# Optimization experiments

Measured on AMD Instinct MI355X. Metric: run time of the kernel, lower is better.

The kernel has to match this reference:

```python
import jax, jax.numpy as jnp
import numpy as np

HEADS = 16
EPS = 1e-6

def _rmsnorm(x, g):
    # x: (..., d); norm = ||x||_2 * d^-0.5 (matches torch.norm-based RMSNorm)
    d = x.shape[-1]
    nrm = jnp.linalg.norm(x, axis=-1, keepdims=True) * (d ** -0.5)
    return x / (nrm + EPS) * g

def _rope(x, cos, sin):
    # x: (b,n,h,d) -> complex pairs over last dim; cos/sin: (1,n,1,d//2)
    b, n, h, d = x.shape
    xr = x.reshape(b, n, h, d // 2, 2)
    re, im = xr[..., 0], xr[..., 1]
    out_re = re * cos - im * sin
    out_im = re * sin + im * cos
    return jnp.stack([out_re, out_im], axis=-1).reshape(b, n, h, d)

def setup_inputs() -> dict:
    key = jax.random.key(0)
    ks = jax.random.split(key, 8)
    b, n, dim = 4, 4096, 1024
    d = dim // HEADS
    x = jax.random.normal(ks[0], (b, n, dim), dtype=jnp.float32)
    # rope freqs as cos/sin of random angles (broadcast shape 1,n,1,d//2)
    ang = jax.random.uniform(ks[1], (1, n, 1, d // 2), dtype=jnp.float32) * (2 * np.pi)
    freqs_cos = jnp.cos(ang)
    freqs_sin = jnp.sin(ang)
    sc = dim ** -0.5
    w_qkv = jax.random.normal(ks[2], (dim, 3 * dim), dtype=jnp.float32) * sc
    g_q = jnp.ones((d,), dtype=jnp.float32)
    g_k = jnp.ones((d,), dtype=jnp.float32)
    w_proj = jax.random.normal(ks[3], (dim, dim), dtype=jnp.float32) * sc
    b_proj = jnp.zeros((dim,), dtype=jnp.float32)
    return {"x": x, "freqs_cos": freqs_cos, "freqs_sin": freqs_sin,
            "w_qkv": w_qkv, "g_q": g_q, "g_k": g_k,
            "w_proj": w_proj, "b_proj": b_proj}

def reference(x, freqs_cos, freqs_sin, w_qkv, g_q, g_k, w_proj, b_proj):
    b, n, dim = x.shape
    h = HEADS
    d = dim // h
    scale = d ** -0.5
    qkv = x @ w_qkv  # (b,n,3*dim)
    q, k, v = jnp.split(qkv, 3, axis=-1)
    q = q.reshape(b, n, h, d)
    k = k.reshape(b, n, h, d)
    v = v.reshape(b, n, h, d)
    q = _rmsnorm(q, g_q)
    k = _rmsnorm(k, g_k)
    q = _rope(q, freqs_cos, freqs_sin)
    k = _rope(k, freqs_cos, freqs_sin)
    # per-token head-mixing attention: (b,n,h,h)
    attn = jnp.einsum('bnhd,bngd->bnhg', q, k) * scale
    attn = jax.nn.softmax(attn, axis=-1)
    out = jnp.einsum('bnhg,bngd->bnhd', attn, v).reshape(b, n, dim)
    return out @ w_proj + b_proj
```

## Files before the change

kernel.cpp:

```cpp
#include <hip/hip_runtime.h>
#include <hip/hip_bf16.h>
#include <stddef.h>

#define NTOK   16384
#define SEQN   4096
#define DIM    1024
#define K3     3072
#define HEADS  16
#define HD     64

typedef __attribute__((ext_vector_type(8))) short short8;
typedef __attribute__((ext_vector_type(4))) float float4v;

static __device__ __forceinline__ unsigned short f32_to_bf16_bits(float f) {
    unsigned u = __float_as_uint(f);
    unsigned r = u + 0x7fffu + ((u >> 16) & 1u);
    return (unsigned short)(r >> 16);
}
static __device__ __forceinline__ unsigned pack_bf16x2(float lo, float hi) {
    return (unsigned)f32_to_bf16_bits(lo) | ((unsigned)f32_to_bf16_bits(hi) << 16);
}
static __device__ __forceinline__ void unpack_bf16x8(uint4 u, float* f) {
    f[0] = __uint_as_float(u.x << 16); f[1] = __uint_as_float(u.x & 0xffff0000u);
    f[2] = __uint_as_float(u.y << 16); f[3] = __uint_as_float(u.y & 0xffff0000u);
    f[4] = __uint_as_float(u.z << 16); f[5] = __uint_as_float(u.z & 0xffff0000u);
    f[6] = __uint_as_float(u.w << 16); f[7] = __uint_as_float(u.w & 0xffff0000u);
}

typedef const void __attribute__((address_space(1)))* gas_ptr;
typedef void __attribute__((address_space(3)))* las_ptr;
static __device__ __forceinline__ void gload_lds16(const unsigned short* g,
                                                   unsigned short* l) {
    __builtin_amdgcn_global_load_lds((gas_ptr)g, (las_ptr)l, 16, 0, 0);
}

__global__ void cvt_f32_bf16(const float4* __restrict__ in,
                             ushort4* __restrict__ out, int n4) {
    int i = blockIdx.x * blockDim.x + threadIdx.x;
    if (i < n4) {
        float4 v = in[i];
        ushort4 o;
        o.x = f32_to_bf16_bits(v.x);
        o.y = f32_to_bf16_bits(v.y);
        o.z = f32_to_bf16_bits(v.z);
        o.w = f32_to_bf16_bits(v.w);
        out[i] = o;
    }
}

__global__ void transpose_cvt(const float* __restrict__ in,
                              unsigned short* __restrict__ out,
                              int K, int N) {
    __shared__ float t[32][33];
    int n0 = blockIdx.x * 32, k0 = blockIdx.y * 32;
    int tx = threadIdx.x, ty = threadIdx.y;
    #pragma unroll
    for (int r = ty; r < 32; r += 8)
        t[r][tx] = in[(size_t)(k0 + r) * N + n0 + tx];
    __syncthreads();
    #pragma unroll
    for (int r = ty; r < 32; r += 8)
        out[(size_t)(n0 + r) * K + k0 + tx] = f32_to_bf16_bits(t[tx][r]);
}

template<int WITH_BIAS>
__global__ __launch_bounds__(256) void gemm_bf16_128(
    const unsigned short* __restrict__ A,
    const unsigned short* __restrict__ Bt,
    void* __restrict__ Cout,
    const float* __restrict__ bias,
    int M, int N, int K)
{
    __shared__ unsigned short As[128][32];
    __shared__ unsigned short Bs[128][32];

    const int tid  = threadIdx.x;
    const int wave = tid >> 6;
    const int lane = tid & 63;
    const int quad = lane >> 4;
    const int l16  = lane & 15;
    const int waveM = (wave & 1) * 64;
    const int waveN = (wave >> 1) * 64;
    const int rowBase = blockIdx.y * 128;
    const int colBase = blockIdx.x * 128;

    float4v acc[4][4];
    #pragma unroll
    for (int i = 0; i < 4; i++)
        #pragma unroll
        for (int j = 0; j < 4; j++)
            acc[i][j] = (float4v)0.0f;

    const int lrow = lane >> 2;
    const int lcol = (lane & 3) * 8;
    const unsigned short* gA = A  + (size_t)(rowBase + wave * 32 + lrow) * K + lcol;
    const unsigned short* gB = Bt + (size_t)(colBase + wave * 32 + lrow) * K + lcol;
    unsigned short* lA0 = &As[wave * 32][0];
    unsigned short* lA1 = &As[wave * 32 + 16][0];
    unsigned short* lB0 = &Bs[wave * 32][0];
    unsigned short* lB1 = &Bs[wave * 32 + 16][0];
    const size_t k16 = (size_t)16 * K;

    for (int k0 = 0; k0 < K; k0 += 32) {
        __syncthreads();
        gload_lds16(gA + k0,        lA0);
        gload_lds16(gA + k0 + k16,  lA1);
        gload_lds16(gB + k0,        lB0);
        gload_lds16(gB + k0 + k16,  lB1);
        __syncthreads();

        short8 af[4], bf[4];
        #pragma unroll
        for (int i = 0; i < 4; i++)
            af[i] = *(const short8*)&As[waveM + i * 16 + l16][quad * 8];
        #pragma unroll
        for (int j = 0; j < 4; j++)
            bf[j] = *(const short8*)&Bs[waveN + j * 16 + l16][quad * 8];

        #pragma unroll
        for (int i = 0; i < 4; i++)
            #pragma unroll
            for (int j = 0; j < 4; j++)
                acc[i][j] = __builtin_amdgcn_mfma_f32_16x16x32_bf16(
                                af[i], bf[j], acc[i][j], 0, 0, 0);
    }

    #pragma unroll
    for (int i = 0; i < 4; i++) {
        #pragma unroll
        for (int j = 0; j < 4; j++) {
            const int col = colBase + waveN + j * 16 + l16;
            #pragma unroll
            for (int r = 0; r < 4; r++) {
                const int row = rowBase + waveM + i * 16 + quad * 4 + r;
                float v = acc[i][j][r];
                if (WITH_BIAS) {
                    ((float*)Cout)[(size_t)row * N + col] = v + bias[col];
                } else {
                    ((unsigned short*)Cout)[(size_t)row * N + col] =
                        f32_to_bf16_bits(v);
                }
            }
        }
    }
}

__global__ __launch_bounds__(256) void attn_tok(
    const unsigned short* __restrict__ qkv,
    const float* __restrict__ fcos,
    const float* __restrict__ fsin,
    const float* __restrict__ gq,
    const float* __restrict__ gk,
    unsigned short* __restrict__ outb)
{
    __shared__ float kl[4][16][68];
    __shared__ float vl[4][16][68];

    const int tid  = threadIdx.x;
    const int wv   = tid >> 6;
    const int lane = tid & 63;
    const int h    = lane & 15;
    const int p    = lane >> 4;
    const int tok  = blockIdx.x * 4 + wv;
    const int n    = tok & (SEQN - 1);

    const unsigned short* base = qkv + (size_t)tok * K3 + h * 64 + p * 16;
    uint4 qr0 = *(const uint4*)(base);
    uint4 qr1 = *(const uint4*)(base + 8);
    uint4 kr0 = *(const uint4*)(base + DIM);
    uint4 kr1 = *(const uint4*)(base + DIM + 8);
    uint4 vr0 = *(const uint4*)(base + 2 * DIM);
    uint4 vr1 = *(const uint4*)(base + 2 * DIM + 8);

    float q[16], k[16], v[16];
    unpack_bf16x8(qr0, q); unpack_bf16x8(qr1, q + 8);
    unpack_bf16x8(kr0, k); unpack_bf16x8(kr1, k + 8);
    unpack_bf16x8(vr0, v); unpack_bf16x8(vr1, v + 8);

    float ssq = 0.f, ssk = 0.f;
    #pragma unroll
    for (int i = 0; i < 16; i++) { ssq += q[i] * q[i]; ssk += k[i] * k[i]; }
    ssq += __shfl_xor(ssq, 16); ssq += __shfl_xor(ssq, 32);
    ssk += __shfl_xor(ssk, 16); ssk += __shfl_xor(ssk, 32);
    const float sq = 1.0f / (sqrtf(ssq) * 0.125f + 1e-6f);
    const float sk = 1.0f / (sqrtf(ssk) * 0.125f + 1e-6f);

    #pragma unroll
    for (int c = 0; c < 4; c++) {
        float4 gg = *(const float4*)(gq + p * 16 + c * 4);
        float4 gh = *(const float4*)(gk + p * 16 + c * 4);
        q[c*4+0] *= sq * gg.x; q[c*4+1] *= sq * gg.y;
        q[c*4+2] *= sq * gg.z; q[c*4+3] *= sq * gg.w;
        k[c*4+0] *= sk * gh.x; k[c*4+1] *= sk * gh.y;
        k[c*4+2] *= sk * gh.z; k[c*4+3] *= sk * gh.w;
    }

    {
        const float* cb = fcos + n * 32 + p * 8;
        const float* sb = fsin + n * 32 + p * 8;
        float4 c0 = *(const float4*)cb, c1 = *(const float4*)(cb + 4);
        float4 s0 = *(const float4*)sb, s1 = *(const float4*)(sb + 4);
        float cs[8] = {c0.x,c0.y,c0.z,c0.w,c1.x,c1.y,c1.z,c1.w};
        float sn[8] = {s0.x,s0.y,s0.z,s0.w,s1.x,s1.y,s1.z,s1.w};
        #pragma unroll
        for (int j = 0; j < 8; j++) {
            float re = q[2*j], im = q[2*j+1];
            q[2*j]   = re * cs[j] - im * sn[j];
            q[2*j+1] = re * sn[j] + im * cs[j];
            re = k[2*j]; im = k[2*j+1];
            k[2*j]   = re * cs[j] - im * sn[j];
            k[2*j+1] = re * sn[j] + im * cs[j];
        }
    }

    {
        float* krow = &kl[wv][h][p * 16];
        float* vrow = &vl[wv][h][p * 16];
        #pragma unroll
        for (int c = 0; c < 4; c++) {
            *(float4*)(krow + c*4) = make_float4(k[c*4], k[c*4+1], k[c*4+2], k[c*4+3]);
            *(float4*)(vrow + c*4) = make_float4(v[c*4], v[c*4+1], v[c*4+2], v[c*4+3]);
        }
    }

    float s[16];
    #pragma unroll
    for (int g = 0; g < 16; g++) {
        const float* kg = &kl[wv][g][p * 16];
        float4 a0 = *(const float4*)(kg);
        float4 a1 = *(const float4*)(kg + 4);
        float4 a2 = *(const float4*)(kg + 8);
        float4 a3 = *(const float4*)(kg + 12);
        s[g] = q[0]*a0.x + q[1]*a0.y + q[2]*a0.z + q[3]*a0.w
             + q[4]*a1.x + q[5]*a1.y + q[6]*a1.z + q[7]*a1.w
             + q[8]*a2.x + q[9]*a2.y + q[10]*a2.z + q[11]*a2.w
             + q[12]*a3.x + q[13]*a3.y + q[14]*a3.z + q[15]*a3.w;
    }
    #pragma unroll
    for (int g = 0; g < 16; g++) {
        s[g] += __shfl_xor(s[g], 16);
        s[g] += __shfl_xor(s[g], 32);
        s[g] *= 0.125f;
    }

    float m = s[0];
    #pragma unroll
    for (int g = 1; g < 16; g++) m = fmaxf(m, s[g]);
    float sum = 0.f;
    #pragma unroll
    for (int g = 0; g < 16; g++) { s[g] = __expf(s[g] - m); sum += s[g]; }
    const float inv = 1.0f / sum;

    float o[16];
    #pragma unroll
    for (int i = 0; i < 16; i++) o[i] = 0.f;
    #pragma unroll
    for (int g = 0; g < 16; g++) {
        const float pg = s[g] * inv;
        const float* vg = &vl[wv][g][p * 16];
        float4 b0 = *(const float4*)(vg);
        float4 b1 = *(const float4*)(vg + 4);
        float4 b2 = *(const float4*)(vg + 8);
        float4 b3 = *(const float4*)(vg + 12);
        o[0]  += pg * b0.x; o[1]  += pg * b0.y; o[2]  += pg * b0.z; o[3]  += pg * b0.w;
        o[4]  += pg * b1.x; o[5]  += pg * b1.y; o[6]  += pg * b1.z; o[7]  += pg * b1.w;
        o[8]  += pg * b2.x; o[9]  += pg * b2.y; o[10] += pg * b2.z; o[11] += pg * b2.w;
        o[12] += pg * b3.x; o[13] += pg * b3.y; o[14] += pg * b3.z; o[15] += pg * b3.w;
    }

    uint4 r0, r1;
    r0.x = pack_bf16x2(o[0],  o[1]);  r0.y = pack_bf16x2(o[2],  o[3]);
    r0.z = pack_bf16x2(o[4],  o[5]);  r0.w = pack_bf16x2(o[6],  o[7]);
    r1.x = pack_bf16x2(o[8],  o[9]);  r1.y = pack_bf16x2(o[10], o[11]);
    r1.z = pack_bf16x2(o[12], o[13]); r1.w = pack_bf16x2(o[14], o[15]);
    unsigned short* ob = outb + (size_t)tok * DIM + h * 64 + p * 16;
    *(uint4*)(ob)     = r0;
    *(uint4*)(ob + 8) = r1;
}

extern "C" void kernel_launch(void* const* d_in, const int* in_sizes, int n_in,
                              void* d_out, int out_size, void* d_ws, size_t ws_size,
                              hipStream_t stream) {
    const float* x      = (const float*)d_in[0];
    const float* fcos   = (const float*)d_in[1];
    const float* fsin   = (const float*)d_in[2];
    const float* w_qkv  = (const float*)d_in[3];
    const float* g_q    = (const float*)d_in[4];
    const float* g_k    = (const float*)d_in[5];
    const float* w_proj = (const float*)d_in[6];
    const float* b_proj = (const float*)d_in[7];
    float* out = (float*)d_out;

    char* ws = (char*)d_ws;
    unsigned short* xb      = (unsigned short*)(ws);
    unsigned short* wqkvT   = (unsigned short*)(ws + 33554432);
    unsigned short* wprojT  = (unsigned short*)(ws + 39845888);
    unsigned short* qkv     = (unsigned short*)(ws + 41943040);
    unsigned short* attnout = (unsigned short*)(ws + 142606336);
    (void)ws_size; (void)in_sizes; (void)n_in; (void)out_size;

    {
        int n4 = (NTOK * DIM) / 4;
        cvt_f32_bf16<<<(n4 + 255) / 256, 256, 0, stream>>>(
            (const float4*)x, (ushort4*)xb, n4);
        transpose_cvt<<<dim3(K3 / 32, DIM / 32), dim3(32, 8), 0, stream>>>(
            w_qkv, wqkvT, DIM, K3);
        transpose_cvt<<<dim3(DIM / 32, DIM / 32), dim3(32, 8), 0, stream>>>(
            w_proj, wprojT, DIM, DIM);
    }
    gemm_bf16_128<0><<<dim3(K3 / 128, NTOK / 128), 256, 0, stream>>>(
        xb, wqkvT, (void*)qkv, nullptr, NTOK, K3, DIM);
    attn_tok<<<NTOK / 4, 256, 0, stream>>>(qkv, fcos, fsin, g_q, g_k, attnout);
    gemm_bf16_128<1><<<dim3(DIM / 128, NTOK / 128), 256, 0, stream>>>(
        attnout, wprojT, (void*)out, b_proj, NTOK, DIM, DIM);
}
```

Baseline: 381.0 us.

## Double-buffer GEMM LDS tiles per wave with vmcnt waits instead of block barriers

Replaces the 128x128 four-wave GEMM with a 64x128 two-wave block in which each wave owns private double-buffered LDS tiles for A and B. The next k-slice is prefetched with direct global-to-LDS loads while the current one feeds the MFMAs. Block-wide syncthreads are replaced by per-wave vmcnt waits, since no data is shared between waves. The cost is that each wave loads its own copy of the A tile, which doubles A traffic and halves reuse per block. It also relies on the global-to-LDS loads being tracked by vmcnt and on the exact wait count matching the number of outstanding loads.

```diff
diff --git a/kernel.cpp b/kernel.cpp
--- a/kernel.cpp
+++ b/kernel.cpp
@@ -11,6 +11,8 @@
 
 typedef __attribute__((ext_vector_type(8))) short short8;
 typedef __attribute__((ext_vector_type(4))) float float4v;
+
+#define WAIT_VMCNT(n) (((n) & 0xF) | (((n) >> 4) << 14) | (0x7 << 4) | (0xF << 8))
 
 static __device__ __forceinline__ unsigned short f32_to_bf16_bits(float f) {
     unsigned u = __float_as_uint(f);
@@ -64,25 +66,22 @@
 }
 
 template<int WITH_BIAS>
-__global__ __launch_bounds__(256) void gemm_bf16_128(
+__global__ __launch_bounds__(128, 2) void gemm_bf16_pipe(
     const unsigned short* __restrict__ A,
     const unsigned short* __restrict__ Bt,
     void* __restrict__ Cout,
     const float* __restrict__ bias,
     int M, int N, int K)
 {
-    __shared__ unsigned short As[128][32];
-    __shared__ unsigned short Bs[128][32];
+    __shared__ unsigned short lds[2][2][2][64][32];
 
     const int tid  = threadIdx.x;
-    const int wave = tid >> 6;
+    const int wv   = tid >> 6;
     const int lane = tid & 63;
     const int quad = lane >> 4;
     const int l16  = lane & 15;
-    const int waveM = (wave & 1) * 64;
-    const int waveN = (wave >> 1) * 64;
-    const int rowBase = blockIdx.y * 128;
-    const int colBase = blockIdx.x * 128;
+    const int rowBase = blockIdx.y * 64;
+    const int colBase = blockIdx.x * 128 + wv * 64;
 
     float4v acc[4][4];
     #pragma unroll
@@ -93,29 +92,39 @@
 
     const int lrow = lane >> 2;
     const int lcol = (lane & 3) * 8;
-    const unsigned short* gA = A  + (size_t)(rowBase + wave * 32 + lrow) * K + lcol;
-    const unsigned short* gB = Bt + (size_t)(colBase + wave * 32 + lrow) * K + lcol;
-    unsigned short* lA0 = &As[wave * 32][0];
-    unsigned short* lA1 = &As[wave * 32 + 16][0];
-    unsigned short* lB0 = &Bs[wave * 32][0];
-    unsigned short* lB1 = &Bs[wave * 32 + 16][0];
+    const unsigned short* gA = A  + (size_t)(rowBase + lrow) * K + lcol;
+    const unsigned short* gB = Bt + (size_t)(colBase + lrow) * K + lcol;
     const size_t k16 = (size_t)16 * K;
 
-    for (int k0 = 0; k0 < K; k0 += 32) {
-        __syncthreads();
-        gload_lds16(gA + k0,        lA0);
-        gload_lds16(gA + k0 + k16,  lA1);
-        gload_lds16(gB + k0,        lB0);
-        gload_lds16(gB + k0 + k16,  lB1);
-        __syncthreads();
+    const int nsteps = K >> 5;
+    int buf = 0;
+
+    #pragma unroll
+    for (int g = 0; g < 4; g++) {
+        gload_lds16(gA + (size_t)g * k16, &lds[wv][0][0][g * 16][0]);
+        gload_lds16(gB + (size_t)g * k16, &lds[wv][0][1][g * 16][0]);
+    }
+
+    for (int s = 0; s + 1 < nsteps; s++) {
+        const size_t k0 = (size_t)(s + 1) << 5;
+        const int nb = buf ^ 1;
+        #pragma unroll
+        for (int g = 0; g < 4; g++) {
+            gload_lds16(gA + k0 + (size_t)g * k16, &lds[wv][nb][0][g * 16][0]);
+            gload_lds16(gB + k0 + (size_t)g * k16, &lds[wv][nb][1][g * 16][0]);
+        }
+
+        __builtin_amdgcn_sched_barrier(0);
+        __builtin_amdgcn_s_waitcnt(WAIT_VMCNT(8));
+        __builtin_amdgcn_sched_barrier(0);
 
         short8 af[4], bf[4];
         #pragma unroll
         for (int i = 0; i < 4; i++)
-            af[i] = *(const short8*)&As[waveM + i * 16 + l16][quad * 8];
+            af[i] = *(const short8*)&lds[wv][buf][0][i * 16 + l16][quad * 8];
         #pragma unroll
         for (int j = 0; j < 4; j++)
-            bf[j] = *(const short8*)&Bs[waveN + j * 16 + l16][quad * 8];
+            bf[j] = *(const short8*)&lds[wv][buf][1][j * 16 + l16][quad * 8];
 
         #pragma unroll
         for (int i = 0; i < 4; i++)
@@ -123,16 +132,38 @@
             for (int j = 0; j < 4; j++)
                 acc[i][j] = __builtin_amdgcn_mfma_f32_16x16x32_bf16(
                                 af[i], bf[j], acc[i][j], 0, 0, 0);
+        buf ^= 1;
+    }
+
+    {
+        __builtin_amdgcn_sched_barrier(0);
+        __builtin_amdgcn_s_waitcnt(WAIT_VMCNT(0));
+        __builtin_amdgcn_sched_barrier(0);
+
+        short8 af[4], bf[4];
+        #pragma unroll
+        for (int i = 0; i < 4; i++)
+            af[i] = *(const short8*)&lds[wv][buf][0][i * 16 + l16][quad * 8];
+        #pragma unroll
+        for (int j = 0; j < 4; j++)
+            bf[j] = *(const short8*)&lds[wv][buf][1][j * 16 + l16][quad * 8];
+
+        #pragma unroll
+        for (int i = 0; i < 4; i++)
+            #pragma unroll
+            for (int j = 0; j < 4; j++)
+                acc[i][j] = __builtin_amdgcn_mfma_f32_16x16x32_bf16(
+                                af[i], bf[j], acc[i][j], 0, 0, 0);
     }
 
     #pragma unroll
     for (int i = 0; i < 4; i++) {
         #pragma unroll
         for (int j = 0; j < 4; j++) {
-            const int col = colBase + waveN + j * 16 + l16;
+            const int col = colBase + j * 16 + l16;
             #pragma unroll
             for (int r = 0; r < 4; r++) {
-                const int row = rowBase + waveM + i * 16 + quad * 4 + r;
+                const int row = rowBase + i * 16 + quad * 4 + r;
                 float v = acc[i][j][r];
                 if (WITH_BIAS) {
                     ((float*)Cout)[(size_t)row * N + col] = v + bias[col];
@@ -308,9 +339,9 @@
         transpose_cvt<<<dim3(DIM / 32, DIM / 32), dim3(32, 8), 0, stream>>>(
             w_proj, wprojT, DIM, DIM);
     }
-    gemm_bf16_128<0><<<dim3(K3 / 128, NTOK / 128), 256, 0, stream>>>(
+    gemm_bf16_pipe<0><<<dim3(K3 / 128, NTOK / 64), 128, 0, stream>>>(
         xb, wqkvT, (void*)qkv, nullptr, NTOK, K3, DIM);
     attn_tok<<<NTOK / 4, 256, 0, stream>>>(qkv, fcos, fsin, g_q, g_k, attnout);
-    gemm_bf16_128<1><<<dim3(DIM / 128, NTOK / 128), 256, 0, stream>>>(
+    gemm_bf16_pipe<1><<<dim3(DIM / 128, NTOK / 64), 128, 0, stream>>>(
         attnout, wprojT, (void*)out, b_proj, NTOK, DIM, DIM);
 }
```

After: 469.0 us. 23.1% more time.

## Use 32x32x16 MFMA with K=64 LDS tiles and XOR swizzle in GEMMs

Applied to the files above, without the earlier changes.

The bf16 GEMM now stages a 64-wide K slice per iteration instead of 32, which halves the number of barrier pairs. It switches from 16x16x32 to 32x32x16 MFMA instructions, giving each wave a 2x2 grid of 32x32 accumulators. LDS rows are XOR-swizzled by row index to avoid bank conflicts on the wider tile rows. This raises LDS use to 32KB per block and changes the output write pattern, which may affect occupancy and store coalescing.

```diff
diff --git a/kernel.cpp b/kernel.cpp
--- a/kernel.cpp
+++ b/kernel.cpp
@@ -9,8 +9,8 @@
 #define HEADS  16
 #define HD     64
 
-typedef __attribute__((ext_vector_type(8))) short short8;
-typedef __attribute__((ext_vector_type(4))) float float4v;
+typedef __attribute__((ext_vector_type(8)))  short  short8;
+typedef __attribute__((ext_vector_type(16))) float  float16v;
 
 static __device__ __forceinline__ unsigned short f32_to_bf16_bits(float f) {
     unsigned u = __float_as_uint(f);
@@ -64,75 +64,72 @@
 }
 
 template<int WITH_BIAS>
-__global__ __launch_bounds__(256) void gemm_bf16_128(
+__global__ __launch_bounds__(256) void gemm_bf16_k64(
     const unsigned short* __restrict__ A,
     const unsigned short* __restrict__ Bt,
     void* __restrict__ Cout,
     const float* __restrict__ bias,
     int M, int N, int K)
 {
-    __shared__ unsigned short As[128][32];
-    __shared__ unsigned short Bs[128][32];
+    __shared__ unsigned short As[128][64];
+    __shared__ unsigned short Bs[128][64];
 
     const int tid  = threadIdx.x;
     const int wave = tid >> 6;
     const int lane = tid & 63;
-    const int quad = lane >> 4;
-    const int l16  = lane & 15;
+    const int l32  = lane & 31;
+    const int hi   = lane >> 5;
+    const int l7   = lane & 7;
     const int waveM = (wave & 1) * 64;
     const int waveN = (wave >> 1) * 64;
     const int rowBase = blockIdx.y * 128;
     const int colBase = blockIdx.x * 128;
 
-    float4v acc[4][4];
-    #pragma unroll
-    for (int i = 0; i < 4; i++)
-        #pragma unroll
-        for (int j = 0; j < 4; j++)
-            acc[i][j] = (float4v)0.0f;
-
-    const int lrow = lane >> 2;
-    const int lcol = (lane & 3) * 8;
-    const unsigned short* gA = A  + (size_t)(rowBase + wave * 32 + lrow) * K + lcol;
-    const unsigned short* gB = Bt + (size_t)(colBase + wave * 32 + lrow) * K + lcol;
-    unsigned short* lA0 = &As[wave * 32][0];
-    unsigned short* lA1 = &As[wave * 32 + 16][0];
-    unsigned short* lB0 = &Bs[wave * 32][0];
-    unsigned short* lB1 = &Bs[wave * 32 + 16][0];
-    const size_t k16 = (size_t)16 * K;
-
-    for (int k0 = 0; k0 < K; k0 += 32) {
+    float16v acc[2][2];
+    #pragma unroll
+    for (int i = 0; i < 2; i++)
+        #pragma unroll
+        for (int j = 0; j < 2; j++)
+            acc[i][j] = (float16v)0.0f;
+
+    const int drow = lane >> 3;
+    const int lc   = l7 ^ drow;
+    const unsigned short* gA = A  + (size_t)(rowBase + wave * 32 + drow) * K + lc * 8;
+    const unsigned short* gB = Bt + (size_t)(colBase + wave * 32 + drow) * K + lc * 8;
+    const size_t k8 = (size_t)8 * K;
+
+    for (int k0 = 0; k0 < K; k0 += 64) {
         __syncthreads();
-        gload_lds16(gA + k0,        lA0);
-        gload_lds16(gA + k0 + k16,  lA1);
-        gload_lds16(gB + k0,        lB0);
-        gload_lds16(gB + k0 + k16,  lB1);
+        #pragma unroll
+        for (int g = 0; g < 4; g++) {
+            gload_lds16(gA + k0 + (size_t)g * k8, &As[wave * 32 + g * 8][0]);
+            gload_lds16(gB + k0 + (size_t)g * k8, &Bs[wave * 32 + g * 8][0]);
+        }
         __syncthreads();
 
-        short8 af[4], bf[4];
-        #pragma unroll
-        for (int i = 0; i < 4; i++)
-            af[i] = *(const short8*)&As[waveM + i * 16 + l16][quad * 8];
-        #pragma unroll
-        for (int j = 0; j < 4; j++)
-            bf[j] = *(const short8*)&Bs[waveN + j * 16 + l16][quad * 8];
-
-        #pragma unroll
-        for (int i = 0; i < 4; i++)
+        #pragma unroll
+        for (int t = 0; t < 4; t++) {
+            const int pc = ((2 * t + hi) ^ l7) * 8;
+            short8 a0 = *(const short8*)&As[waveM + l32][pc];
+            short8 a1 = *(const short8*)&As[waveM + 32 + l32][pc];
+            short8 b0 = *(const short8*)&Bs[waveN + l32][pc];
+            short8 b1 = *(const short8*)&Bs[waveN + 32 + l32][pc];
+            acc[0][0] = __builtin_amdgcn_mfma_f32_32x32x16_bf16(a0, b0, acc[0][0], 0, 0, 0);
+            acc[0][1] = __builtin_amdgcn_mfma_f32_32x32x16_bf16(a0, b1, acc[0][1], 0, 0, 0);
+            acc[1][0] = __builtin_amdgcn_mfma_f32_32x32x16_bf16(a1, b0, acc[1][0], 0, 0, 0);
+            acc[1][1] = __builtin_amdgcn_mfma_f32_32x32x16_bf16(a1, b1, acc[1][1], 0, 0, 0);
+        }
+    }
+
+    #pragma unroll
+    for (int i = 0; i < 2; i++) {
+        #pragma unroll
+        for (int j = 0; j < 2; j++) {
+            const int col = colBase + waveN + j * 32 + l32;
             #pragma unroll
-            for (int j = 0; j < 4; j++)
-                acc[i][j] = __builtin_amdgcn_mfma_f32_16x16x32_bf16(
-                                af[i], bf[j], acc[i][j], 0, 0, 0);
-    }
-
-    #pragma unroll
-    for (int i = 0; i < 4; i++) {
-        #pragma unroll
-        for (int j = 0; j < 4; j++) {
-            const int col = colBase + waveN + j * 16 + l16;
-            #pragma unroll
-            for (int r = 0; r < 4; r++) {
-                const int row = rowBase + waveM + i * 16 + quad * 4 + r;
+            for (int r = 0; r < 16; r++) {
+                const int row = rowBase + waveM + i * 32
+                              + (r & 3) + 8 * (r >> 2) + 4 * hi;
                 float v = acc[i][j][r];
                 if (WITH_BIAS) {
                     ((float*)Cout)[(size_t)row * N + col] = v + bias[col];
@@ -308,9 +305,9 @@
         transpose_cvt<<<dim3(DIM / 32, DIM / 32), dim3(32, 8), 0, stream>>>(
             w_proj, wprojT, DIM, DIM);
     }
-    gemm_bf16_128<0><<<dim3(K3 / 128, NTOK / 128), 256, 0, stream>>>(
+    gemm_bf16_k64<0><<<dim3(K3 / 128, NTOK / 128), 256, 0, stream>>>(
         xb, wqkvT, (void*)qkv, nullptr, NTOK, K3, DIM);
     attn_tok<<<NTOK / 4, 256, 0, stream>>>(qkv, fcos, fsin, g_q, g_k, attnout);
-    gemm_bf16_128<1><<<dim3(DIM / 128, NTOK / 128), 256, 0, stream>>>(
+    gemm_bf16_k64<1><<<dim3(DIM / 128, NTOK / 128), 256, 0, stream>>>(
         attnout, wprojT, (void*)out, b_proj, NTOK, DIM, DIM);
 }
```

Result: faster. 361.2 us (-5.2%).
